# Performance work log

Hardware: AMD Instinct MI355X
Metric: run time of the kernel (lower is better)

The kernel has to match this reference:

```python
import jax, jax.numpy as jnp
import numpy as np

B, C, H, W = 16, 256, 64, 64
OUT_C = 3
N_TOKENS = 512
N_RES = 3
RED = 4
CB = C // RED  # bottleneck channels in ResChain
DN = ('NCHW', 'OIHW', 'NCHW')


def _conv(x, w, pad):
    return jax.lax.conv_general_dilated(x, w, (1, 1), pad, dimension_numbers=DN)


def setup_inputs() -> dict:
    key = jax.random.key(0)
    ks = jax.random.split(key, 8)
    return {
        'input': jax.random.normal(ks[0], (B, C, H, W), jnp.float32),
        'embed': jax.random.normal(ks[1], (C, N_TOKENS), jnp.float32),  # Quantize codebook [dim, n_embed]
        'res_w1': jax.random.normal(ks[2], (N_RES, CB, C, 3, 3), jnp.float32) * 0.02,
        'res_b1': jnp.zeros((N_RES, CB), jnp.float32),
        'res_w2': jax.random.normal(ks[3], (N_RES, C, CB, 1, 1), jnp.float32) * 0.02,
        'res_b2': jnp.zeros((N_RES, C), jnp.float32),
        'out_w': jax.random.normal(ks[4], (OUT_C, C, 1, 1), jnp.float32) * 0.02,
        'out_b': jnp.zeros((OUT_C,), jnp.float32),
    }


def reference(input, embed, res_w1, res_b1, res_w2, res_b2, out_w, out_b):
    sg = jax.lax.stop_gradient
    # --- Quantize (VQ-VAE codebook lookup, straight-through) ---
    x = jnp.transpose(input, (0, 2, 3, 1))  # [B,H,W,C]
    flat = x.reshape(-1, C)                  # [N, C]
    # squared L2 distance to each code: ||f||^2 - 2 f.e + ||e||^2
    dist = (flat * flat).sum(-1, keepdims=True) - 2.0 * (flat @ embed) + (embed * embed).sum(0)
    idx = jnp.argmin(dist, axis=-1).reshape(B, H, W)        # [B,H,W] int
    quantize = jnp.take(embed.T, idx, axis=0)               # embed_code: [B,H,W,C]
    diff = jnp.mean((sg(quantize) - x) ** 2)
    quantize = x + sg(quantize - x)                         # straight-through
    q = jnp.transpose(quantize, (0, 3, 1, 2))               # [B,C,H,W]
    # --- dec: ResChain(n_res_block) + 1x1 conv ---
    for i in range(N_RES):
        h = jax.nn.relu(q)
        h = _conv(h, res_w1[i], 'SAME') + res_b1[i][None, :, None, None]
        h = jax.nn.relu(h)
        h = _conv(h, res_w2[i], 'VALID') + res_b2[i][None, :, None, None]
        q = q + h
    quant = _conv(q, out_w, 'VALID') + out_b[None, :, None, None]  # [B,OUT_C,H,W]
    # --- wordfreq: per-batch bincount over idx (no grad) ---
    flat_idx = idx.reshape(B, -1)
    seg = (flat_idx + jnp.arange(B, dtype=flat_idx.dtype)[:, None] * N_TOKENS).reshape(-1)
    counts = jax.ops.segment_sum(jnp.ones_like(seg, jnp.float32), seg, num_segments=B * N_TOKENS)
    wordfreq = counts.reshape(B, N_TOKENS) / float(H * W)
    return quant, diff.reshape(1), wordfreq
```

## Files before the change

kernel.cpp:

```cpp
#include <hip/hip_runtime.h>


typedef __attribute__((ext_vector_type(8))) short short8;
typedef __attribute__((ext_vector_type(16))) float f32x16;
typedef __attribute__((ext_vector_type(8))) _Float16 half8;
typedef __attribute__((ext_vector_type(2))) _Float16 half2_t;
typedef unsigned short ushort_t;
typedef unsigned long long u64;

#define WS_QA    0
#define WS_QB    8388608
#define WS_ET    16777216
#define WS_EN    16842752
#define WS_EPK   16843264
#define WS_W1PK  16908800
#define WS_W2PK  17129984
#define WS_DIFF  17154560
#define WS_TOK   17154568
#define WS_DST   17220104
#define WS_FN    17285640
#define WS_WL    17351176

#define MARGIN 0.12f

__device__ inline ushort_t f2bf(float f) {
  unsigned u = __float_as_uint(f);
  return (ushort_t)((u + 0x7fffu + ((u >> 16) & 1u)) >> 16);
}
__device__ inline float bf2f(ushort_t h) { return __uint_as_float(((unsigned)h) << 16); }
union HU { _Float16 h; ushort_t u; };
union S8H { short8 s; half8 h; half2_t h2[4]; };

__global__ __launch_bounds__(256) void prep_kernel(
    const float* __restrict__ embed, const float* __restrict__ w1,
    const float* __restrict__ w2, float* __restrict__ ws, float* __restrict__ wf) {
  int i = blockIdx.x * 256 + threadIdx.x;
  if (i < 131072) {
    int t = i >> 8, c = i & 255;
    ((ushort_t*)(ws + WS_ET))[i] = f2bf(embed[c * 512 + t]);
  }
  if (i < 512) {
    float s = 0.f;
    for (int c = 0; c < 256; ++c) { float v = embed[c * 512 + i]; s += v * v; }
    ws[WS_EN + i] = s;
  }
  if (i < 131072) {
    int j = i & 7, lane = (i >> 3) & 63, at = (i >> 9) & 15, ks = i >> 13;
    int code = at * 32 + (lane & 31);
    int c = ks * 16 + (lane >> 5) * 8 + j;
    HU cv; cv.h = (_Float16)embed[c * 512 + code];
    ((ushort_t*)(ws + WS_EPK))[i] = cv.u;
  }
  if (i < 442368) {
    int j = i & 7; int lane = (i >> 3) & 63; int of = (i >> 9) & 1;
    int k16 = (i >> 10) & 15; int rest = i >> 14;
    int tap = rest % 9; int layer = rest / 9;
    int oc = of * 32 + (lane & 31);
    int c = k16 * 16 + (lane >> 5) * 8 + j;
    ((ushort_t*)(ws + WS_W1PK))[i] = f2bf(w1[((layer * 64 + oc) * 256 + c) * 9 + tap]);
  }
  if (i < 49152) {
    int j = i & 7, lane = (i >> 3) & 63, at = (i >> 9) & 7, ks = (i >> 12) & 3, l = i >> 14;
    int co = at * 32 + (lane & 31), cb = ks * 16 + (lane >> 5) * 8 + j;
    ((ushort_t*)(ws + WS_W2PK))[i] = f2bf(w2[(l * 256 + co) * 64 + cb]);
  }
  if (i < 8192) wf[i] = 0.f;
  if (i == 0) { ws[WS_DIFF] = 0.f; ((int*)(ws + WS_WL))[0] = 0; }
}

__global__ __launch_bounds__(512, 4) void dist_kernel(
    const float* __restrict__ input, const half8* __restrict__ epk,
    const float* __restrict__ enorm, int* __restrict__ tok,
    float* __restrict__ dst, float* __restrict__ fnv, int* __restrict__ wl) {
  __shared__ __align__(16) ushort_t sfp[2048 * 8];
  __shared__ float senorm[512];
  __shared__ float trim1[512], trim2[512];
  __shared__ int   trii[512];

  int blk = blockIdx.x, b = blk >> 6, hw0 = (blk & 63) << 6;
  int tid = threadIdx.x, lane = tid & 63, wave = tid >> 6;
  senorm[tid] = enorm[tid];

  {
    int cg = tid >> 3, sub = tid & 7;
    int ks_s = cg >> 2, hi_s = (cg >> 1) & 1, jq = cg & 1;
    const float* src0 = input + ((size_t)(b * 256 + cg * 4)) * 4096 + hw0 + sub * 8;
    float vv[4][8];
#pragma unroll
    for (int m = 0; m < 4; ++m) {
      const float4* s4 = (const float4*)(src0 + (size_t)m * 4096);
      float4 aa = s4[0], bb = s4[1];
      vv[m][0] = aa.x; vv[m][1] = aa.y; vv[m][2] = aa.z; vv[m][3] = aa.w;
      vv[m][4] = bb.x; vv[m][5] = bb.y; vv[m][6] = bb.z; vv[m][7] = bb.w;
    }
    u64* sfp64 = (u64*)sfp;
#pragma unroll
    for (int i = 0; i < 8; ++i) {
      int pl = sub * 8 + i;
      int bt = pl >> 5, lw = (pl & 31) + 32 * hi_s;
      u64 pk = 0;
#pragma unroll
      for (int m = 0; m < 4; ++m) {
        HU cv; cv.h = (_Float16)vv[m][i];
        pk |= ((u64)cv.u) << (16 * m);
      }
      sfp64[((bt * 16 + ks_s) * 64 + lw) * 2 + jq] = pk;
    }
  }
  __syncthreads();

  f32x16 acc[2][2];
#pragma unroll
  for (int bt = 0; bt < 2; ++bt)
#pragma unroll
    for (int a = 0; a < 2; ++a)
#pragma unroll
      for (int r = 0; r < 16; ++r) acc[bt][a][r] = 0.f;

  const short8* sfp8 = (const short8*)sfp;
  float fnp0 = 0.f, fnp1 = 0.f;
#pragma unroll 2
  for (int ks = 0; ks < 16; ++ks) {
    S8H u0, u1;
    u0.s = sfp8[ks * 64 + lane];
    u1.s = sfp8[(16 + ks) * 64 + lane];
#if __has_builtin(__builtin_amdgcn_fdot2)
#pragma unroll
    for (int k = 0; k < 4; ++k) {
      fnp0 = __builtin_amdgcn_fdot2(u0.h2[k], u0.h2[k], fnp0, false);
      fnp1 = __builtin_amdgcn_fdot2(u1.h2[k], u1.h2[k], fnp1, false);
    }
#else
#pragma unroll
    for (int k = 0; k < 8; ++k) {
      float v0 = (float)u0.h[k], v1 = (float)u1.h[k];
      fnp0 += v0 * v0; fnp1 += v1 * v1;
    }
#endif
#pragma unroll
    for (int a = 0; a < 2; ++a) {
      half8 ah = epk[(ks * 16 + wave * 2 + a) * 64 + lane];
      acc[0][a] = __builtin_amdgcn_mfma_f32_32x32x16_f16(ah, u0.h, acc[0][a], 0, 0, 0);
      acc[1][a] = __builtin_amdgcn_mfma_f32_32x32x16_f16(ah, u1.h, acc[1][a], 0, 0, 0);
    }
  }
  fnp0 += __shfl_xor(fnp0, 32, 64);
  fnp1 += __shfl_xor(fnp1, 32, 64);

  int hi5 = lane >> 5;
#pragma unroll
  for (int bt = 0; bt < 2; ++bt) {
    float m1 = 3.4e38f, m2 = 3.4e38f; int i1 = 0;
#pragma unroll
    for (int a = 0; a < 2; ++a)
#pragma unroll
      for (int r = 0; r < 16; ++r) {
        int code = (wave * 2 + a) * 32 + (r & 3) + 8 * (r >> 2) + 4 * hi5;
        float v = senorm[code] - 2.0f * acc[bt][a][r];
        if (v < m1) { m2 = m1; m1 = v; i1 = code; }
        else if (v < m2) m2 = v;
      }
    float o1 = __shfl_xor(m1, 32, 64);
    float o2 = __shfl_xor(m2, 32, 64);
    int   oi = __shfl_xor(i1, 32, 64);
    float n2 = fminf(fmaxf(m1, o1), fminf(m2, o2));
    float n1 = fminf(m1, o1);
    int   ni = (o1 < m1) ? oi : i1;
    if (lane < 32) {
      int p = bt * 32 + lane;
      trim1[p * 8 + wave] = n1; trim2[p * 8 + wave] = n2; trii[p * 8 + wave] = ni;
    }
  }
  __syncthreads();

  if (wave == 0) {
    int p = lane;
    float m1 = trim1[p * 8], m2 = trim2[p * 8]; int i1 = trii[p * 8];
#pragma unroll
    for (int w = 1; w < 8; ++w) {
      float a1 = trim1[p * 8 + w], a2 = trim2[p * 8 + w]; int ai = trii[p * 8 + w];
      float n2 = fminf(fmaxf(m1, a1), fminf(m2, a2));
      if (a1 < m1) { m1 = a1; i1 = ai; }
      m2 = n2;
    }
    float myfn = (lane < 32) ? fnp0 : fnp1;
    int gpos = blk * 64 + p;
    tok[gpos] = i1;
    dst[gpos] = myfn + m1;
    fnv[gpos] = myfn;
    bool flag = (m2 - m1 < MARGIN);
    u64 mk = __ballot(flag);
    int base = 0;
    if (lane == 0 && mk) base = atomicAdd(wl, (int)__popcll(mk));
    base = __shfl(base, 0, 64);
    if (flag) {
      int off = (int)__popcll(mk & ((1ull << lane) - 1ull));
      wl[1 + base + off] = gpos;
    }
  }
}

__global__ __launch_bounds__(256) void redo_kernel(
    const float* __restrict__ input, const float* __restrict__ embed,
    const float* __restrict__ enorm, const int* __restrict__ wl,
    int* __restrict__ tok, float* __restrict__ dst, const float* __restrict__ fnv) {
  __shared__ float sf[256], rv[256];
  __shared__ int   ri[256];
  int n = wl[0];
  int tid = threadIdx.x;
  for (int e = blockIdx.x; e < n; e += gridDim.x) {
    int gpos = wl[1 + e];
    int b = gpos >> 12, hw = gpos & 4095;
    sf[tid] = input[((size_t)(b * 256 + tid)) * 4096 + hw];
    __syncthreads();
    float d0 = 0.f, d1 = 0.f;
#pragma unroll 4
    for (int c = 0; c < 256; ++c) {
      float fv = sf[c];
      d0 += fv * embed[c * 512 + tid];
      d1 += fv * embed[c * 512 + 256 + tid];
    }
    float v0 = enorm[tid] - 2.f * d0;
    float v1 = enorm[256 + tid] - 2.f * d1;
    float bv; int bi;
    if (v1 < v0) { bv = v1; bi = 256 + tid; } else { bv = v0; bi = tid; }
    rv[tid] = bv; ri[tid] = bi;
    __syncthreads();
    for (int s = 128; s > 0; s >>= 1) {
      if (tid < s) {
        float ov = rv[tid + s]; int oi2 = ri[tid + s];
        if (ov < rv[tid] || (ov == rv[tid] && oi2 < ri[tid])) { rv[tid] = ov; ri[tid] = oi2; }
      }
      __syncthreads();
    }
    if (tid == 0) { tok[gpos] = ri[0]; dst[gpos] = fnv[gpos] + rv[0]; }
    __syncthreads();
  }
}

__global__ __launch_bounds__(256) void finalize_kernel(
    const int* __restrict__ tok, const float* __restrict__ dst,
    const ushort_t* __restrict__ embedT, float* __restrict__ wf,
    float* __restrict__ diffp, ushort_t* __restrict__ qout) {
  int blk = blockIdx.x;
  int tid = threadIdx.x, lane = tid & 63, wave = tid >> 6;
  int gbase = blk * 64;
  int b = gbase >> 12;
  if (wave == 0) {
    int t = tok[gbase + lane];
    atomicAdd(&wf[b * 512 + t], 1.0f / 4096.0f);
    float d = dst[gbase + lane];
#pragma unroll
    for (int off = 32; off >= 1; off >>= 1) d += __shfl_down(d, off, 64);
    if (lane == 0) atomicAdd(diffp, d);
  }
#pragma unroll 1
  for (int j = 0; j < 16; ++j) {
    int p = wave * 16 + j;
    int t = __builtin_amdgcn_readfirstlane(tok[gbase + p]);
    const u64* src = (const u64*)(embedT + (size_t)t * 256);
    u64* dstp = (u64*)(qout + ((size_t)(gbase + p)) * 256);
    dstp[lane] = src[lane];
  }
}

__global__ __launch_bounds__(256, 4) void fused_layer(
    const ushort_t* __restrict__ qin, ushort_t* __restrict__ qout,
    const ushort_t* __restrict__ w1pk, const float* __restrict__ b1,
    const ushort_t* __restrict__ w2pk, const float* __restrict__ b2, int l) {
  __shared__ __align__(16) char arena[28160];
  ushort_t* hbuf   = (ushort_t*)arena;
  float*    sb2    = (float*)(arena + 9728);
  short8*   stg    = (short8*)(arena + 10752);
  ushort_t* qstage = (ushort_t*)(arena + 10752);

  int blk = blockIdx.x;
  int b = blk >> 6; int t = blk & 63;
  int ty0 = (t >> 3) << 3;
  int tx0 = (t & 7) << 3;
  int tid = threadIdx.x, lane = tid & 63, w = tid >> 6;
  int pt = w & 1, ot = w >> 1;
  int l31 = lane & 31, kb5 = lane >> 5;

  sb2[tid] = b2[l * 256 + tid];

  const short8* wp  = (const short8*)w1pk + (size_t)l * 18432;
  const short8* w2p = (const short8*)w2pk;

  auto stage = [&](int cs, int buf) {
#pragma unroll
    for (int e = 0; e < 2; ++e) {
      int u = e * 256 + tid;
      if (u < 400) {
        int cg = u & 3; int pix = u >> 2; int y = pix / 10; int x = pix - y * 10;
        int sy = ty0 + y - 1, sx = tx0 + x - 1;
        short8 sv;
        if (sy >= 0 && sy < 64 && sx >= 0 && sx < 64) {
          sv = *(const short8*)(qin + ((size_t)(b * 4096 + sy * 64 + sx)) * 256 + cs * 32 + cg * 8);
#pragma unroll
          for (int k2 = 0; k2 < 8; ++k2) if (sv[k2] < 0) sv[k2] = 0;
        } else {
#pragma unroll
          for (int k2 = 0; k2 < 8; ++k2) sv[k2] = 0;
        }
        stg[buf * 440 + (y * 4 + cg) * 11 + x] = sv;
      }
    }
  };

  f32x16 acc;
#pragma unroll
  for (int r = 0; r < 16; ++r) acc[r] = 0.f;

  int py0 = pt * 4 + (l31 >> 3);
  int px0 = lane & 7;

  stage(0, 0);
  __syncthreads();
#pragma unroll 1
  for (int cs = 0; cs < 8; ++cs) {
    if (cs < 7) stage(cs + 1, (cs + 1) & 1);
    int buf = cs & 1;
#pragma unroll 1
    for (int dy = 0; dy < 3; ++dy) {
#pragma unroll 1
      for (int dx = 0; dx < 3; ++dx) {
        int tap = dy * 3 + dx;
#pragma unroll
        for (int ks2 = 0; ks2 < 2; ++ks2) {
          short8 A = stg[buf * 440 + ((py0 + dy) * 4 + ks2 * 2 + kb5) * 11 + px0 + dx];
          short8 B = wp[(tap * 16 + cs * 2 + ks2) * 128 + ot * 64 + lane];
          acc = __builtin_amdgcn_mfma_f32_32x32x16_bf16(A, B, acc, 0, 0, 0);
        }
      }
    }
    __syncthreads();
  }

  {
    int oc = ot * 32 + l31;
    float bb = b1[l * 64 + oc];
#pragma unroll
    for (int r = 0; r < 16; ++r) {
      int row = (r & 3) + 8 * (r >> 2) + 4 * kb5;
      hbuf[(pt * 32 + row) * 76 + oc] = f2bf(fmaxf(acc[r] + bb, 0.f));
    }
  }
  __syncthreads();

  int pt2 = w & 1, coq = w >> 1;
#pragma unroll 1
  for (int ch = 0; ch < 2; ++ch) {
    f32x16 acc2[2];
#pragma unroll
    for (int a = 0; a < 2; ++a)
#pragma unroll
      for (int r = 0; r < 16; ++r) acc2[a][r] = 0.f;

#pragma unroll
    for (int ks = 0; ks < 4; ++ks) {
      short8 A = *(const short8*)(hbuf + (pt2 * 32 + l31) * 76 + ks * 16 + kb5 * 8);
#pragma unroll
      for (int a = 0; a < 2; ++a) {
        short8 B = w2p[((l * 4 + ks) * 8 + ch * 4 + coq * 2 + a) * 64 + lane];
        acc2[a] = __builtin_amdgcn_mfma_f32_32x32x16_bf16(A, B, acc2[a], 0, 0, 0);
      }
    }
#pragma unroll
    for (int a = 0; a < 2; ++a) {
      int cc = coq * 64 + a * 32 + l31;
      float bb2 = sb2[ch * 128 + cc];
#pragma unroll
      for (int r = 0; r < 16; ++r) {
        int row = (r & 3) + 8 * (r >> 2) + 4 * kb5;
        qstage[(pt2 * 32 + row) * 136 + cc] = f2bf(acc2[a][r] + bb2);
      }
    }
    __syncthreads();
#pragma unroll
    for (int it = 0; it < 4; ++it) {
      int u = it * 256 + tid;
      int p = u >> 4, c8 = u & 15;
      short8 hv = *(const short8*)(qstage + p * 136 + c8 * 8);
      int gy = ty0 + (p >> 3), gx = tx0 + (p & 7);
      size_t gidx = ((size_t)(b * 4096 + gy * 64 + gx)) * 256 + ch * 128 + c8 * 8;
      short8 qv = *(const short8*)(qin + gidx);
      short8 ov;
#pragma unroll
      for (int k2 = 0; k2 < 8; ++k2)
        ov[k2] = (short)f2bf(bf2f((ushort_t)qv[k2]) + bf2f((ushort_t)hv[k2]));
      *(short8*)(qout + gidx) = ov;
    }
    __syncthreads();
  }
}

__global__ __launch_bounds__(256) void final_kernel(
    const ushort_t* __restrict__ qbuf, const float* __restrict__ ow,
    const float* __restrict__ ob, float* __restrict__ out,
    const float* __restrict__ ws) {
  int t = blockIdx.x * 256 + threadIdx.x;
  int pos = t >> 4, c16 = t & 15;
  const ushort_t* qp = qbuf + (size_t)pos * 256 + c16 * 16;
  short8 v0 = *(const short8*)qp;
  short8 v1 = *(const short8*)(qp + 8);
  float a0 = 0.f, a1 = 0.f, a2 = 0.f;
#pragma unroll
  for (int k = 0; k < 16; ++k) {
    float f = bf2f((ushort_t)(k < 8 ? v0[k] : v1[k - 8]));
    int c = c16 * 16 + k;
    a0 += f * ow[c];
    a1 += f * ow[256 + c];
    a2 += f * ow[512 + c];
  }
#pragma unroll
  for (int off = 1; off < 16; off <<= 1) {
    a0 += __shfl_xor(a0, off, 64);
    a1 += __shfl_xor(a1, off, 64);
    a2 += __shfl_xor(a2, off, 64);
  }
  if (c16 == 0) {
    int b = pos >> 12, hw = pos & 4095;
    out[(b * 3 + 0) * 4096 + hw] = a0 + ob[0];
    out[(b * 3 + 1) * 4096 + hw] = a1 + ob[1];
    out[(b * 3 + 2) * 4096 + hw] = a2 + ob[2];
  }
  if (t == 0) out[196608] = ws[WS_DIFF] * (1.0f / 16777216.0f);
}

extern "C" void kernel_launch(void* const* d_in, const int* in_sizes, int n_in,
                              void* d_out, int out_size, void* d_ws, size_t ws_size,
                              hipStream_t stream) {
  (void)in_sizes; (void)n_in; (void)out_size; (void)ws_size;
  const float* input = (const float*)d_in[0];
  const float* embed = (const float*)d_in[1];
  const float* b1 = (const float*)d_in[3];
  const float* b2 = (const float*)d_in[5];
  const float* ow = (const float*)d_in[6];
  const float* ob = (const float*)d_in[7];
  float* ws = (float*)d_ws;
  float* out = (float*)d_out;
  float* wf = out + 196609;

  ushort_t* qA = (ushort_t*)(ws + WS_QA);
  ushort_t* qB = (ushort_t*)(ws + WS_QB);
  const ushort_t* et = (const ushort_t*)(ws + WS_ET);
  const half8* epk = (const half8*)(ws + WS_EPK);
  const ushort_t* w1pk = (const ushort_t*)(ws + WS_W1PK);
  const ushort_t* w2pk = (const ushort_t*)(ws + WS_W2PK);
  int*   tok = (int*)(ws + WS_TOK);
  float* dst = ws + WS_DST;
  float* fnv = ws + WS_FN;
  int*   wl  = (int*)(ws + WS_WL);

  hipLaunchKernelGGL(prep_kernel, dim3(1728), dim3(256), 0, stream,
                     embed, (const float*)d_in[2], (const float*)d_in[4], ws, wf);
  hipLaunchKernelGGL(dist_kernel, dim3(1024), dim3(512), 0, stream,
                     input, epk, ws + WS_EN, tok, dst, fnv, wl);
  hipLaunchKernelGGL(redo_kernel, dim3(1024), dim3(256), 0, stream,
                     input, embed, ws + WS_EN, wl, tok, dst, fnv);
  hipLaunchKernelGGL(finalize_kernel, dim3(1024), dim3(256), 0, stream,
                     tok, dst, et, wf, ws + WS_DIFF, qA);
  hipLaunchKernelGGL(fused_layer, dim3(1024), dim3(256), 0, stream,
                     qA, qB, w1pk, b1, w2pk, b2, 0);
  hipLaunchKernelGGL(fused_layer, dim3(1024), dim3(256), 0, stream,
                     qB, qA, w1pk, b1, w2pk, b2, 1);
  hipLaunchKernelGGL(fused_layer, dim3(1024), dim3(256), 0, stream,
                     qA, qB, w1pk, b1, w2pk, b2, 2);
  hipLaunchKernelGGL(final_kernel, dim3(4096), dim3(256), 0, stream,
                     qB, ow, ob, out, ws);
}
```

Baseline: 231.2 us.

## Prefetch conv input chunks into registers and widen K-chunk to 64 channels

The 3x3 conv staging now loads the next 64-channel chunk into registers before the MFMA loop and writes it to LDS afterwards, so global load latency overlaps with compute. It halves the number of chunk iterations and barriers, and doubles the LDS staging buffers to hold 64 channels. The residual input for the second stage is prefetched into registers before the 1x1 MFMA work. The larger LDS footprint and extra registers may reduce occupancy below the launch-bounds target.

```diff
diff --git a/kernel.cpp b/kernel.cpp
--- a/kernel.cpp
+++ b/kernel.cpp
@@ -268,7 +268,7 @@
     const ushort_t* __restrict__ qin, ushort_t* __restrict__ qout,
     const ushort_t* __restrict__ w1pk, const float* __restrict__ b1,
     const ushort_t* __restrict__ w2pk, const float* __restrict__ b2, int l) {
-  __shared__ __align__(16) char arena[28160];
+  __shared__ __align__(16) char arena[38912];
   ushort_t* hbuf   = (ushort_t*)arena;
   float*    sb2    = (float*)(arena + 9728);
   short8*   stg    = (short8*)(arena + 10752);
@@ -287,23 +287,35 @@
   const short8* wp  = (const short8*)w1pk + (size_t)l * 18432;
   const short8* w2p = (const short8*)w2pk;
 
-  auto stage = [&](int cs, int buf) {
-#pragma unroll
-    for (int e = 0; e < 2; ++e) {
-      int u = e * 256 + tid;
-      if (u < 400) {
-        int cg = u & 3; int pix = u >> 2; int y = pix / 10; int x = pix - y * 10;
+  short8 sreg[4];
+  auto loadch = [&](int cs) {
+#pragma unroll
+    for (int s = 0; s < 4; ++s) {
+      int u = s * 256 + tid;
+      if (u < 800) {
+        int cg = u & 7; int pix = u >> 3; int y = pix / 10; int x = pix - y * 10;
         int sy = ty0 + y - 1, sx = tx0 + x - 1;
-        short8 sv;
         if (sy >= 0 && sy < 64 && sx >= 0 && sx < 64) {
-          sv = *(const short8*)(qin + ((size_t)(b * 4096 + sy * 64 + sx)) * 256 + cs * 32 + cg * 8);
-#pragma unroll
-          for (int k2 = 0; k2 < 8; ++k2) if (sv[k2] < 0) sv[k2] = 0;
+          sreg[s] = *(const short8*)(qin + ((size_t)(b * 4096 + sy * 64 + sx)) * 256 + cs * 64 + cg * 8);
         } else {
-#pragma unroll
-          for (int k2 = 0; k2 < 8; ++k2) sv[k2] = 0;
+          short8 z;
+#pragma unroll
+          for (int k2 = 0; k2 < 8; ++k2) z[k2] = 0;
+          sreg[s] = z;
         }
-        stg[buf * 440 + (y * 4 + cg) * 11 + x] = sv;
+      }
+    }
+  };
+  auto writech = [&](int buf) {
+#pragma unroll
+    for (int s = 0; s < 4; ++s) {
+      int u = s * 256 + tid;
+      if (u < 800) {
+        int cg = u & 7; int pix = u >> 3; int y = pix / 10; int x = pix - y * 10;
+        short8 sv = sreg[s];
+#pragma unroll
+        for (int k2 = 0; k2 < 8; ++k2) if (sv[k2] < 0) sv[k2] = 0;
+        stg[buf * 880 + (y * 8 + cg) * 11 + x] = sv;
       }
     }
   };
@@ -315,11 +327,12 @@
   int py0 = pt * 4 + (l31 >> 3);
   int px0 = lane & 7;
 
-  stage(0, 0);
-  __syncthreads();
+  loadch(0);
+  writech(0);
 #pragma unroll 1
-  for (int cs = 0; cs < 8; ++cs) {
-    if (cs < 7) stage(cs + 1, (cs + 1) & 1);
+  for (int cs = 0; cs < 4; ++cs) {
+    __syncthreads();
+    if (cs < 3) loadch(cs + 1);
     int buf = cs & 1;
 #pragma unroll 1
     for (int dy = 0; dy < 3; ++dy) {
@@ -327,15 +340,16 @@
       for (int dx = 0; dx < 3; ++dx) {
         int tap = dy * 3 + dx;
 #pragma unroll
-        for (int ks2 = 0; ks2 < 2; ++ks2) {
-          short8 A = stg[buf * 440 + ((py0 + dy) * 4 + ks2 * 2 + kb5) * 11 + px0 + dx];
-          short8 B = wp[(tap * 16 + cs * 2 + ks2) * 128 + ot * 64 + lane];
+        for (int ks2 = 0; ks2 < 4; ++ks2) {
+          short8 A = stg[buf * 880 + ((py0 + dy) * 8 + ks2 * 2 + kb5) * 11 + px0 + dx];
+          short8 B = wp[(tap * 16 + cs * 4 + ks2) * 128 + ot * 64 + lane];
           acc = __builtin_amdgcn_mfma_f32_32x32x16_bf16(A, B, acc, 0, 0, 0);
         }
       }
     }
-    __syncthreads();
-  }
+    if (cs < 3) writech((cs + 1) & 1);
+  }
+  __syncthreads();
 
   {
     int oc = ot * 32 + l31;
@@ -351,6 +365,15 @@
   int pt2 = w & 1, coq = w >> 1;
 #pragma unroll 1
   for (int ch = 0; ch < 2; ++ch) {
+    short8 qv[4];
+#pragma unroll
+    for (int it = 0; it < 4; ++it) {
+      int u = it * 256 + tid;
+      int p = u >> 4, c8 = u & 15;
+      int gy = ty0 + (p >> 3), gx = tx0 + (p & 7);
+      qv[it] = *(const short8*)(qin + ((size_t)(b * 4096 + gy * 64 + gx)) * 256 + ch * 128 + c8 * 8);
+    }
+
     f32x16 acc2[2];
 #pragma unroll
     for (int a = 0; a < 2; ++a)
@@ -384,11 +407,10 @@
       short8 hv = *(const short8*)(qstage + p * 136 + c8 * 8);
       int gy = ty0 + (p >> 3), gx = tx0 + (p & 7);
       size_t gidx = ((size_t)(b * 4096 + gy * 64 + gx)) * 256 + ch * 128 + c8 * 8;
-      short8 qv = *(const short8*)(qin + gidx);
       short8 ov;
 #pragma unroll
       for (int k2 = 0; k2 < 8; ++k2)
-        ov[k2] = (short)f2bf(bf2f((ushort_t)qv[k2]) + bf2f((ushort_t)hv[k2]));
+        ov[k2] = (short)f2bf(bf2f((ushort_t)qv[it][k2]) + bf2f((ushort_t)hv[k2]));
       *(short8*)(qout + gidx) = ov;
     }
     __syncthreads();
```

New measurement: 239.4 us. 1.04x slower.
